# Performance work log

Measured on AMD Instinct MI355X. Metric: run time of the kernel, lower is better.

Reference implementation:

```python
import jax, jax.numpy as jnp
import numpy as np

D_MODEL = 768
D_STATE = 16
D_CONV = 4
EXPAND = 2
D_INNER = D_MODEL * EXPAND
B, L = 2, 2048


def _silu(x):
    return x * jax.nn.sigmoid(x)


def _ssm_core(xn, inw, cw, cb, xw, dtw, dtb, Alog, Dp, outw):
    """Mamba selective SSM. xn: [B,L,d_model] -> [B,L,d_model]."""
    Bn, Ln, _ = xn.shape
    S = Alog.shape[1]
    d_inner = Alog.shape[0]
    k = cw.shape[-1]
    xz = xn @ inw                      # [B,L,2*d_inner]
    xi, z = jnp.split(xz, 2, axis=-1)
    # depthwise causal conv along L (torch pads both sides then slices [:L] == left-pad k-1)
    xc = jnp.swapaxes(xi, 1, 2)        # [B,d_inner,L]
    xc = jax.lax.conv_general_dilated(xc, cw, (1,), [(k - 1, 0)],
                                      feature_group_count=d_inner)
    xc = xc + cb[None, :, None]
    xc = _silu(jnp.swapaxes(xc, 1, 2))  # [B,L,d_inner]
    bcdt = xc @ xw                     # [B,L,1+2S]
    dt_raw = bcdt[..., :1]
    Bs = bcdt[..., 1:1 + S]            # [B,L,S]
    Cs = bcdt[..., 1 + S:]             # [B,L,S]
    dt = jax.nn.softplus(dt_raw * dtw[None, None, :] + dtb)  # [B,L,d_inner]
    A = -jnp.exp(jnp.clip(Alog, -6.0, 6.0))                  # [d_inner,S]
    dA = jnp.exp(dt[..., None] * A[None, None])               # [B,L,d_inner,S]
    dBx = dt[..., None] * Bs[:, :, None, :] * xc[..., None]   # [B,L,d_inner,S]

    def step(h, ins):
        dA_t, dBx_t, C_t = ins
        h = jnp.clip(dA_t * h + dBx_t, -10000.0, 10000.0)
        return h, jnp.einsum('bds,bs->bd', h, C_t)

    h0 = jnp.zeros((Bn, d_inner, S), xc.dtype)
    _, ys = jax.lax.scan(step, h0, (jnp.moveaxis(dA, 1, 0),
                                    jnp.moveaxis(dBx, 1, 0),
                                    jnp.moveaxis(Cs, 1, 0)))
    y = jnp.moveaxis(ys, 0, 1) + xc * Dp[None, None]
    y = y * _silu(z)
    return y @ outw


def setup_inputs() -> dict:
    key = jax.random.key(0)
    ks = jax.random.split(key, 20)
    def core_params(koff):
        return dict(
            inw=jax.random.normal(ks[koff + 0], (D_MODEL, 2 * D_INNER), jnp.float32) * 0.02,
            cw=jax.random.normal(ks[koff + 1], (D_INNER, 1, D_CONV), jnp.float32) * 0.2,
            cb=jnp.zeros((D_INNER,), jnp.float32),
            xw=jax.random.normal(ks[koff + 2], (D_INNER, 1 + 2 * D_STATE), jnp.float32) * 0.02,
            dtw=jax.random.normal(ks[koff + 3], (D_INNER,), jnp.float32) * 0.5,
            dtb=jax.random.normal(ks[koff + 4], (D_INNER,), jnp.float32) * 0.1,
            Alog=jnp.clip(jnp.log(jnp.arange(1, D_STATE + 1, dtype=jnp.float32))[None, :]
                          * jnp.ones((D_INNER, 1), jnp.float32), -6.0, 6.0),
            D=jnp.ones((D_INNER,), jnp.float32),
            outw=jax.random.normal(ks[koff + 5], (D_INNER, D_MODEL), jnp.float32) * 0.02,
        )
    f = core_params(2)
    b = core_params(8)
    return {
        'x': jax.random.normal(ks[0], (B, L, D_MODEL), jnp.float32),
        'ln_g': jnp.ones((D_MODEL,), jnp.float32),
        'ln_b': jnp.zeros((D_MODEL,), jnp.float32),
        'alpha': jnp.zeros((), jnp.float32),
        'f_inw': f['inw'], 'f_cw': f['cw'], 'f_cb': f['cb'], 'f_xw': f['xw'],
        'f_dtw': f['dtw'], 'f_dtb': f['dtb'], 'f_Alog': f['Alog'], 'f_D': f['D'], 'f_outw': f['outw'],
        'b_inw': b['inw'], 'b_cw': b['cw'], 'b_cb': b['cb'], 'b_xw': b['xw'],
        'b_dtw': b['dtw'], 'b_dtb': b['dtb'], 'b_Alog': b['Alog'], 'b_D': b['D'], 'b_outw': b['outw'],
    }


def reference(x, ln_g, ln_b, alpha,
              f_inw, f_cw, f_cb, f_xw, f_dtw, f_dtb, f_Alog, f_D, f_outw,
              b_inw, b_cw, b_cb, b_xw, b_dtw, b_dtb, b_Alog, b_D, b_outw):
    residual = x.astype(jnp.float32)
    mu = residual.mean(-1, keepdims=True)
    var = ((residual - mu) ** 2).mean(-1, keepdims=True)
    xn = (residual - mu) / jnp.sqrt(var + 1e-5) * ln_g + ln_b
    y_fwd = _ssm_core(xn, f_inw, f_cw, f_cb, f_xw, f_dtw, f_dtb, f_Alog, f_D, f_outw)
    y_bwd = jnp.flip(_ssm_core(jnp.flip(xn, 1), b_inw, b_cw, b_cb, b_xw,
                               b_dtw, b_dtb, b_Alog, b_D, b_outw), 1)
    a = jax.nn.sigmoid(alpha)
    y = a * y_fwd + (1.0 - a) * y_bwd
    return y + residual
```

## Files before the change

### kernel.cpp

```cpp
#include <hip/hip_runtime.h>
#include <cstddef>
#include <cstdint>

#define DMODEL 768
#define DINNER 1536
#define NSTATE 16
#define LSEQ   2048
#define NB     2
#define NTOK   (NB*LSEQ)
#define NBCDT  33

#define TC     32
#define NCHUNK (LSEQ/TC)
#define KSPLIT 12
#define LOG2E  1.44269504f

typedef __bf16 bf16x8 __attribute__((ext_vector_type(8)));
typedef float  floatx4 __attribute__((ext_vector_type(4)));

__device__ __forceinline__ float exp2_hw(float x) { return __builtin_amdgcn_exp2f(x); }
__device__ __forceinline__ float silu_f(float x) { return x / (1.f + expf(-x)); }
__device__ __forceinline__ float clip1e4(float x) {
    return __builtin_amdgcn_fmed3f(x, -1e4f, 1e4f);
}
__device__ __forceinline__ unsigned short f2bf(float f) {
    unsigned int u = __float_as_uint(f);
    unsigned int r = u + 0x7fffu + ((u >> 16) & 1u);
    return (unsigned short)(r >> 16);
}
__device__ __forceinline__ float bf2f(unsigned short u) {
    return __uint_as_float((unsigned int)u << 16);
}
__device__ __forceinline__ unsigned int pack2bf(float a, float b) {
    unsigned int ua = __float_as_uint(a); ua = ua + 0x7fffu + ((ua >> 16) & 1u);
    unsigned int ub = __float_as_uint(b); ub = ub + 0x7fffu + ((ub >> 16) & 1u);
    return (ua >> 16) | (ub & 0xffff0000u);
}
__device__ __forceinline__ void ld_lds16(unsigned short* lds, const unsigned short* g) {
    __builtin_amdgcn_global_load_lds(
        (const __attribute__((address_space(1))) unsigned int*)g,
        (__attribute__((address_space(3))) unsigned int*)lds,
        16, 0, 0);
}

__global__ void ln_kernel(const float* __restrict__ x,
                          const float* __restrict__ g,
                          const float* __restrict__ be,
                          unsigned short* __restrict__ xnb,
                          float* __restrict__ bcdt,
                          float* __restrict__ out) {
    int row = blockIdx.x;
    int tid = threadIdx.x;
    int zi = row * 256 + tid;
    if (zi < 2 * NTOK * NBCDT) bcdt[zi] = 0.f;
    const float* xr = x + (size_t)row * DMODEL;
    float s = 0.f, ss = 0.f;
    for (int i = tid; i < DMODEL; i += 256) {
        float v = xr[i];
        s += v; ss += v * v;
    }
    for (int o = 32; o >= 1; o >>= 1) {
        s  += __shfl_xor(s,  o, 64);
        ss += __shfl_xor(ss, o, 64);
    }
    __shared__ float sS[4], sSS[4];
    int w = tid >> 6;
    if ((tid & 63) == 0) { sS[w] = s; sSS[w] = ss; }
    __syncthreads();
    s  = sS[0] + sS[1] + sS[2] + sS[3];
    ss = sSS[0] + sSS[1] + sSS[2] + sSS[3];
    float mu = s / DMODEL;
    float var = ss / DMODEL - mu * mu;
    float rstd = rsqrtf(var + 1e-5f);
    unsigned short* xo = xnb + (size_t)row * DMODEL;
    float* ores = out + (size_t)row * DMODEL;
    for (int i = tid; i < DMODEL; i += 256) {
        float v = xr[i];
        xo[i] = f2bf((v - mu) * rstd * g[i] + be[i]);
        ores[i] = v;
    }
}

__global__ __launch_bounds__(256)
void cast_weights(const float* __restrict__ f_inw, const float* __restrict__ b_inw,
                  const float* __restrict__ f_outw, const float* __restrict__ b_outw,
                  const float* __restrict__ f_xw, const float* __restrict__ b_xw,
                  const float* __restrict__ alpha,
                  unsigned short* __restrict__ inwT, unsigned short* __restrict__ outwT,
                  unsigned short* __restrict__ xwT) {
    __shared__ float t[32][33];
    int bid = blockIdx.x;
    int tid = threadIdx.x;
    int lr = tid >> 5, lc = tid & 31;
    if (bid < 4608) {
        int n0 = (bid % 192) * 32;
        int k0 = (bid / 192) * 32;
        const float* w = (n0 >= 3072) ? b_inw : f_inw;
        int nb = (n0 >= 3072) ? (n0 - 3072) : n0;
        #pragma unroll
        for (int r = 0; r < 4; r++)
            t[r * 8 + lr][lc] = w[(size_t)(k0 + r * 8 + lr) * 3072 + nb + lc];
        __syncthreads();
        #pragma unroll
        for (int r = 0; r < 4; r++)
            inwT[(size_t)(n0 + r * 8 + lr) * DMODEL + k0 + lc] = f2bf(t[lc][r * 8 + lr]);
    } else if (bid < 6912) {
        bid -= 4608;
        float a = 1.f / (1.f + expf(-alpha[0]));
        int n0 = (bid % 24) * 32;
        int k0 = (bid / 24) * 32;
        const float* w = (k0 >= DINNER) ? b_outw : f_outw;
        float sc = (k0 >= DINNER) ? (1.f - a) : a;
        int kb = (k0 >= DINNER) ? (k0 - DINNER) : k0;
        #pragma unroll
        for (int r = 0; r < 4; r++)
            t[r * 8 + lr][lc] = w[(size_t)(kb + r * 8 + lr) * DMODEL + n0 + lc];
        __syncthreads();
        #pragma unroll
        for (int r = 0; r < 4; r++)
            outwT[(size_t)(n0 + r * 8 + lr) * 3072 + k0 + lc] = f2bf(sc * t[lc][r * 8 + lr]);
    } else {
        bid -= 6912;
        int dir = bid / 48;
        int k0 = (bid % 48) * 32;
        const float* xw = dir ? b_xw : f_xw;
        unsigned short* dst = xwT + (size_t)dir * 48 * DINNER;
        for (int idx = tid; idx < 48 * 32; idx += 256) {
            int n = idx >> 5, kk = idx & 31;
            float v = (n < 33) ? xw[(size_t)(k0 + kk) * 33 + n] : 0.f;
            dst[(size_t)n * DINNER + k0 + kk] = f2bf(v);
        }
    }
}

__global__ __launch_bounds__(256)
void gemm_xz_mfma(const unsigned short* __restrict__ xnb,
                  const unsigned short* __restrict__ inwT,
                  unsigned short* __restrict__ xi, unsigned short* __restrict__ sz) {
    __shared__ unsigned short SH[2][2 * 128 * 64];
    int tid = threadIdx.x;
    int bm = blockIdx.y * 128;
    int bn = blockIdx.x * 128;
    int wave = tid >> 6, lane = tid & 63;
    int wm = (wave & 1) * 64, wn = (wave >> 1) * 64;
    int col15 = lane & 15, quad = lane >> 4;
    int lrow = lane >> 3;
    int lk   = (((lane & 7) ^ lrow) * 8);
    floatx4 acc[4][4];
    #pragma unroll
    for (int i = 0; i < 4; i++)
        #pragma unroll
        for (int j = 0; j < 4; j++)
            acc[i][j] = (floatx4){0.f, 0.f, 0.f, 0.f};

    int sw = col15 & 7;

#define STAGE_XZ(buf, k0)                                                       \
    {                                                                           \
        unsigned short* Abuf = SH[buf];                                         \
        unsigned short* Bbuf = SH[buf] + 128 * 64;                              \
        _Pragma("unroll")                                                       \
        for (int i = 0; i < 4; i++) {                                           \
            int r8 = wave * 32 + i * 8;                                         \
            int ra = r8 + lrow;                                                 \
            ld_lds16(&Abuf[r8 * 64], &xnb[(size_t)(bm + ra) * DMODEL + (k0) + lk]); \
            ld_lds16(&Bbuf[r8 * 64], &inwT[(size_t)(bn + ra) * DMODEL + (k0) + lk]); \
        }                                                                       \
    }

    STAGE_XZ(0, 0);
    __syncthreads();
    int cur = 0;
    for (int kt = 0; kt < DMODEL / 64; ++kt) {
        if (kt + 1 < DMODEL / 64) STAGE_XZ(cur ^ 1, (kt + 1) * 64);
        const unsigned short* Acur = SH[cur];
        const unsigned short* Bcur = SH[cur] + 128 * 64;
        #pragma unroll
        for (int k2 = 0; k2 < 2; k2++) {
            bf16x8 af[4], bf_[4];
            int pc = ((k2 * 4 + quad) ^ sw) * 8;
            #pragma unroll
            for (int mt = 0; mt < 4; mt++)
                af[mt] = *(const bf16x8*)(&Acur[(wm + mt * 16 + col15) * 64 + pc]);
            #pragma unroll
            for (int nt = 0; nt < 4; nt++)
                bf_[nt] = *(const bf16x8*)(&Bcur[(wn + nt * 16 + col15) * 64 + pc]);
            #pragma unroll
            for (int mt = 0; mt < 4; mt++)
                #pragma unroll
                for (int nt = 0; nt < 4; nt++)
                    acc[mt][nt] = __builtin_amdgcn_mfma_f32_16x16x32_bf16(
                        af[mt], bf_[nt], acc[mt][nt], 0, 0, 0);
        }
        __syncthreads();
        cur ^= 1;
    }
    int dirq = (bn >= 3072) ? 1 : 0;
    int cb0  = bn - dirq * 3072;
    int zs   = (cb0 >= DINNER) ? 1 : 0;
    int ccb  = cb0 - zs * DINNER;
    unsigned short* dst = zs ? sz : xi;
    unsigned short* C16 = &SH[0][0];
    #pragma unroll
    for (int mt = 0; mt < 4; mt++)
        #pragma unroll
        for (int nt = 0; nt < 4; nt++)
            #pragma unroll
            for (int r = 0; r < 4; r++) {
                int row = wm + mt * 16 + quad * 4 + r;
                int col = wn + nt * 16 + col15;
                float v = acc[mt][nt][r];
                if (zs) v = silu_f(v);
                C16[row * 136 + col] = f2bf(v);
            }
    __syncthreads();
    {
        int erow = tid >> 4;
        int cch  = tid & 15;
        size_t rowbase = (size_t)dirq * NTOK + bm;
        #pragma unroll
        for (int p = 0; p < 8; p++) {
            int row = p * 16 + erow;
            uint4 v = *(const uint4*)(&C16[row * 136 + cch * 8]);
            *(uint4*)(&dst[(rowbase + row) * DINNER + ccb + cch * 8]) = v;
        }
    }
#undef STAGE_XZ
}

__global__ __launch_bounds__(256)
void bcdt_conv_gemm_mfma(const unsigned short* __restrict__ xi,
                         const float* __restrict__ f_cw, const float* __restrict__ f_cb,
                         const float* __restrict__ b_cw, const float* __restrict__ b_cb,
                         const unsigned short* __restrict__ xwT,
                         float* __restrict__ bcdt) {
    __shared__ unsigned short Xs[131 * 64];
    __shared__ unsigned short As[128 * 64];
    __shared__ unsigned short Bs[48 * 64];
    int tid = threadIdx.x;
    int wave = tid >> 6, lane = tid & 63;
    int r0 = blockIdx.x * 128;
    int kc = blockIdx.y;
    int dirb = r0 >> 11;
    int dir = dirb >> 1, b = dirb & 1;
    int u0 = r0 & 2047;
    const float* cw = dir ? b_cw : f_cw;
    const float* cb = dir ? b_cb : f_cb;
    size_t xibase = ((size_t)dir * NTOK + (size_t)b * LSEQ) * DINNER;
    const unsigned short* Bsrc = xwT + (size_t)dir * 48 * DINNER;

    int col15 = lane & 15, quad = lane >> 4;
    int sw = col15 & 7;
    int lrow = lane >> 3;
    int lcc = (lane & 7) * 8;
    int lk  = (((lane & 7) ^ lrow) * 8);
    int wm = wave * 32;

    int cp = (tid & 31) * 2;
    int rg = (tid >> 5) * 16;

    floatx4 acc[2][3];
    #pragma unroll
    for (int i = 0; i < 2; i++)
        #pragma unroll
        for (int j = 0; j < 3; j++)
            acc[i][j] = (floatx4){0.f, 0.f, 0.f, 0.f};

    for (int ks = 0; ks < 2; ks++) {
        int kb = kc * 128 + ks * 64;
        #pragma unroll
        for (int i = 0; i < 2; i++) {
            int g = wave + i * 4;
            if (g < 6)
                ld_lds16(&Bs[g * 8 * 64],
                         &Bsrc[(size_t)(g * 8 + lrow) * DINNER + kb + lk]);
        }
        #pragma unroll
        for (int i = 0; i < 4; i++) {
            int g = wave * 4 + i;
            int u = u0 + g * 8 + lrow;
            int l = dir ? (LSEQ - 1 - u) : u;
            ld_lds16(&Xs[(3 + g * 8) * 64], &xi[xibase + (size_t)l * DINNER + kb + lcc]);
        }
        if (tid < 96) {
            int hh = tid >> 5, c2 = (tid & 31) * 2;
            int u = u0 - 3 + hh;
            unsigned int v = 0;
            if (u >= 0) {
                int l = dir ? (LSEQ - 1 - u) : u;
                v = *(const unsigned int*)(&xi[xibase + (size_t)l * DINNER + kb + c2]);
            }
            *(unsigned int*)(&Xs[hh * 64 + c2]) = v;
        }
        __syncthreads();
        {
            int ch0 = kb + cp;
            float4 w0 = *(const float4*)(cw + (size_t)ch0 * 4);
            float4 w1 = *(const float4*)(cw + (size_t)(ch0 + 1) * 4);
            float cb0 = cb[ch0], cb1 = cb[ch0 + 1];
            unsigned int v;
            v = *(const unsigned int*)(&Xs[(rg + 0) * 64 + cp]);
            float a3 = bf2f((unsigned short)v), b3 = bf2f((unsigned short)(v >> 16));
            v = *(const unsigned int*)(&Xs[(rg + 1) * 64 + cp]);
            float a2 = bf2f((unsigned short)v), b2 = bf2f((unsigned short)(v >> 16));
            v = *(const unsigned int*)(&Xs[(rg + 2) * 64 + cp]);
            float a1 = bf2f((unsigned short)v), b1 = bf2f((unsigned short)(v >> 16));
            int cs = cp >> 3, e = cp & 7;
            #pragma unroll
            for (int j = 0; j < 16; j++) {
                int r = rg + j;
                v = *(const unsigned int*)(&Xs[(r + 3) * 64 + cp]);
                float a0 = bf2f((unsigned short)v), b0 = bf2f((unsigned short)(v >> 16));
                float xa = cb0;
                xa = fmaf(w0.x, a3, xa); xa = fmaf(w0.y, a2, xa);
                xa = fmaf(w0.z, a1, xa); xa = fmaf(w0.w, a0, xa);
                xa = silu_f(xa);
                float xb = cb1;
                xb = fmaf(w1.x, b3, xb); xb = fmaf(w1.y, b2, xb);
                xb = fmaf(w1.z, b1, xb); xb = fmaf(w1.w, b0, xb);
                xb = silu_f(xb);
                a3 = a2; a2 = a1; a1 = a0;
                b3 = b2; b2 = b1; b1 = b0;
                int ad = r * 64 + ((cs ^ (r & 7)) << 3) + e;
                *(unsigned int*)(&As[ad]) = pack2bf(xa, xb);
            }
        }
        __syncthreads();
        #pragma unroll
        for (int k2 = 0; k2 < 2; k2++) {
            int pc = ((k2 * 4 + quad) ^ sw) * 8;
            bf16x8 af[2], bfr[3];
            #pragma unroll
            for (int mt = 0; mt < 2; mt++)
                af[mt] = *(const bf16x8*)(&As[(wm + mt * 16 + col15) * 64 + pc]);
            #pragma unroll
            for (int nt = 0; nt < 3; nt++)
                bfr[nt] = *(const bf16x8*)(&Bs[(nt * 16 + col15) * 64 + pc]);
            #pragma unroll
            for (int mt = 0; mt < 2; mt++)
                #pragma unroll
                for (int nt = 0; nt < 3; nt++)
                    acc[mt][nt] = __builtin_amdgcn_mfma_f32_16x16x32_bf16(
                        af[mt], bfr[nt], acc[mt][nt], 0, 0, 0);
        }
        __syncthreads();
    }
    #pragma unroll
    for (int mt = 0; mt < 2; mt++) {
        #pragma unroll
        for (int nt = 0; nt < 3; nt++) {
            int n = nt * 16 + col15;
            if (n < 33) {
                #pragma unroll
                for (int r = 0; r < 4; r++) {
                    int row = r0 + wm + mt * 16 + quad * 4 + r;
                    atomicAdd(&bcdt[(size_t)row * 33 + n], acc[mt][nt][r]);
                }
            }
        }
    }
}

__global__ __launch_bounds__(256)
void scan_p1(const unsigned short* __restrict__ xi, const float* __restrict__ bcdt,
             const float* __restrict__ f_cw, const float* __restrict__ f_cb,
             const float* __restrict__ b_cw, const float* __restrict__ b_cb,
             const float* __restrict__ f_dtw, const float* __restrict__ f_dtb,
             const float* __restrict__ f_Alog,
             const float* __restrict__ b_dtw, const float* __restrict__ b_dtb,
             const float* __restrict__ b_Alog,
             float* __restrict__ Sdtbuf, float* __restrict__ hloc) {
    int tid = threadIdx.x;
    int d = blockIdx.x * 256 + tid;
    int chunk = blockIdx.y;
    int dirb  = blockIdx.z;
    int dir = dirb >> 1, b = dirb & 1;
    const float* dtw  = dir ? b_dtw  : f_dtw;
    const float* dtb  = dir ? b_dtb  : f_dtb;
    const float* Alog = dir ? b_Alog : f_Alog;
    const float* cw   = dir ? b_cw   : f_cw;
    const float* cb   = dir ? b_cb   : f_cb;
    float dtw_d = dtw[d], dtb_d = dtb[d];
    float4 wc = *(const float4*)(cw + (size_t)d * 4);
    float cb_d = cb[d];
    float A2[NSTATE], h[NSTATE];
    #pragma unroll
    for (int s = 0; s < NSTATE; s++) {
        float al = fminf(fmaxf(Alog[d * NSTATE + s], -6.f), 6.f);
        A2[s] = -__expf(al) * LOG2E;
        h[s] = 0.f;
    }
    float Sdt = 0.f;
    int t0 = chunk * TC;
    size_t xbase = ((size_t)dir * NTOK + (size_t)b * LSEQ) * DINNER + d;
    long stride = dir ? -(long)DINNER : (long)DINNER;
    int l0 = dir ? (LSEQ - 1 - t0) : t0;
    const unsigned short* xp = xi + xbase + (size_t)l0 * DINNER;
    float xm3 = 0.f, xm2 = 0.f, xm1 = 0.f;
    if (chunk) {
        xm3 = bf2f(*(xp - 3 * stride));
        xm2 = bf2f(*(xp - 2 * stride));
        xm1 = bf2f(*(xp - 1 * stride));
    }
    size_t rbase = (size_t)dirb * LSEQ + (size_t)t0;
    const float* bc = bcdt + rbase * NBCDT;
    for (int t = 0; t < TC; t++) {
        float cur = bf2f(*xp); xp += stride;
        float xv = cb_d;
        xv = fmaf(wc.x, xm3, xv);
        xv = fmaf(wc.y, xm2, xv);
        xv = fmaf(wc.z, xm1, xv);
        xv = fmaf(wc.w, cur, xv);
        xv = silu_f(xv);
        xm3 = xm2; xm2 = xm1; xm1 = cur;
        float dt_raw = bc[t * NBCDT];
        float u = fmaf(dt_raw, dtw_d, dtb_d);
        float dt = fmaxf(u, 0.f) + __logf(1.f + __expf(-fabsf(u)));
        Sdt += dt;
        float dtx = dt * xv;
        #pragma unroll
        for (int s = 0; s < NSTATE; s++) {
            float Bv = bc[t * NBCDT + 1 + s];
            h[s] = fmaf(exp2_hw(dt * A2[s]), h[s], dtx * Bv);
        }
    }
    Sdtbuf[(size_t)chunk * (4 * DINNER) + (size_t)dirb * DINNER + d] = Sdt;
    size_t base = ((size_t)chunk * 4 + dirb) * ((size_t)DINNER * NSTATE) + (size_t)d * NSTATE;
    #pragma unroll
    for (int s = 0; s < NSTATE; s++)
        hloc[base + s] = h[s];
}

__global__ void scan_p2(const float* __restrict__ Sdtbuf, const float* __restrict__ hloc,
                        const float* __restrict__ f_Alog, const float* __restrict__ b_Alog,
                        float* __restrict__ hin) {
    int i = blockIdx.x * 256 + threadIdx.x;
    const int DS = DINNER * NSTATE;
    int dirb = i / DS;
    int rem = i - dirb * DS;
    int d = rem >> 4, s = rem & 15;
    const float* Alog = (dirb >> 1) ? b_Alog : f_Alog;
    float al = fminf(fmaxf(Alog[d * NSTATE + s], -6.f), 6.f);
    float A2 = -__expf(al) * LOG2E;
    float h = 0.f;
    const int stride = 4 * DS;
    const int sstr = 4 * DINNER;
    for (int c = 0; c < NCHUNK; c++) {
        size_t idx = (size_t)c * stride + i;
        hin[idx] = h;
        float P = exp2_hw(A2 * Sdtbuf[(size_t)c * sstr + dirb * DINNER + d]);
        h = clip1e4(fmaf(P, h, hloc[idx]));
    }
}

__global__ __launch_bounds__(256)
void scan_p3(const unsigned short* __restrict__ xi, const float* __restrict__ bcdt,
             const unsigned short* __restrict__ sz, const float* __restrict__ hin,
             const float* __restrict__ f_cw, const float* __restrict__ f_cb,
             const float* __restrict__ b_cw, const float* __restrict__ b_cb,
             const float* __restrict__ f_dtw, const float* __restrict__ f_dtb,
             const float* __restrict__ f_Alog, const float* __restrict__ f_D,
             const float* __restrict__ b_dtw, const float* __restrict__ b_dtb,
             const float* __restrict__ b_Alog, const float* __restrict__ b_D,
             unsigned short* __restrict__ yvb) {
    int tid = threadIdx.x;
    int d = blockIdx.x * 256 + tid;
    int chunk = blockIdx.y;
    int dirb  = blockIdx.z;
    int dir = dirb >> 1, b = dirb & 1;
    const float* dtw  = dir ? b_dtw  : f_dtw;
    const float* dtb  = dir ? b_dtb  : f_dtb;
    const float* Alog = dir ? b_Alog : f_Alog;
    const float* Dp   = dir ? b_D    : f_D;
    const float* cw   = dir ? b_cw   : f_cw;
    const float* cb   = dir ? b_cb   : f_cb;
    float dtw_d = dtw[d], dtb_d = dtb[d], D_d = Dp[d];
    float4 wc = *(const float4*)(cw + (size_t)d * 4);
    float cb_d = cb[d];
    float A2[NSTATE], h[NSTATE];
    size_t hbase = ((size_t)chunk * 4 + dirb) * ((size_t)DINNER * NSTATE) + (size_t)d * NSTATE;
    #pragma unroll
    for (int s = 0; s < NSTATE; s++) {
        float al = fminf(fmaxf(Alog[d * NSTATE + s], -6.f), 6.f);
        A2[s] = -__expf(al) * LOG2E;
        h[s] = hin[hbase + s];
    }
    int t0 = chunk * TC;
    size_t xbase = ((size_t)dir * NTOK + (size_t)b * LSEQ) * DINNER + d;
    long stride = dir ? -(long)DINNER : (long)DINNER;
    int l0 = dir ? (LSEQ - 1 - t0) : t0;
    const unsigned short* xp = xi + xbase + (size_t)l0 * DINNER;
    const unsigned short* szp = sz + xbase + (size_t)l0 * DINNER;
    unsigned short* yp = yvb + ((size_t)(b * LSEQ + l0)) * 3072 + dir * DINNER + d;
    long ystride = stride * 2;
    float xm3 = 0.f, xm2 = 0.f, xm1 = 0.f;
    if (chunk) {
        xm3 = bf2f(*(xp - 3 * stride));
        xm2 = bf2f(*(xp - 2 * stride));
        xm1 = bf2f(*(xp - 1 * stride));
    }
    size_t rbase = (size_t)dirb * LSEQ + (size_t)t0;
    const float* bc = bcdt + rbase * NBCDT;
    for (int t = 0; t < TC; t++) {
        float cur = bf2f(*xp); xp += stride;
        float xv = cb_d;
        xv = fmaf(wc.x, xm3, xv);
        xv = fmaf(wc.y, xm2, xv);
        xv = fmaf(wc.z, xm1, xv);
        xv = fmaf(wc.w, cur, xv);
        xv = silu_f(xv);
        xm3 = xm2; xm2 = xm1; xm1 = cur;
        float dt_raw = bc[t * NBCDT];
        float u = fmaf(dt_raw, dtw_d, dtb_d);
        float dt = fmaxf(u, 0.f) + __logf(1.f + __expf(-fabsf(u)));
        float dtx = dt * xv;
        float p = 0.f;
        #pragma unroll
        for (int s = 0; s < NSTATE; s++) {
            float Bv = bc[t * NBCDT + 1 + s];
            float Cv = bc[t * NBCDT + 1 + NSTATE + s];
            h[s] = fmaf(exp2_hw(dt * A2[s]), h[s], dtx * Bv);
            p = fmaf(h[s], Cv, p);
        }
        float szv = bf2f(*szp); szp += stride;
        float y = (p + xv * D_d) * szv;
        *yp = f2bf(y); yp += ystride;
    }
}

__global__ __launch_bounds__(256)
void gemm_out_mfma(const unsigned short* __restrict__ yvb,
                   const unsigned short* __restrict__ outwT,
                   float* __restrict__ out) {
    __shared__ unsigned short SH[2][(128 + 64) * 64];
    int tid = threadIdx.x;
    int bm = blockIdx.y * 128;
    int bn = blockIdx.x * 64;
    int ks = blockIdx.z;
    int wave = tid >> 6, lane = tid & 63;
    int wm = (wave & 1) * 64, wn = (wave >> 1) * 32;
    int col15 = lane & 15, quad = lane >> 4;
    int lrow = lane >> 3;
    int lk   = (((lane & 7) ^ lrow) * 8);
    floatx4 acc[4][2];
    #pragma unroll
    for (int i = 0; i < 4; i++)
        #pragma unroll
        for (int j = 0; j < 2; j++)
            acc[i][j] = (floatx4){0.f, 0.f, 0.f, 0.f};

    int sw = col15 & 7;
    int kbase = ks * DINNER;

#define STAGE_OUT(buf, k0)                                                      \
    {                                                                           \
        unsigned short* Abuf = SH[buf];                                         \
        unsigned short* Bbuf = SH[buf] + 128 * 64;                              \
        _Pragma("unroll")                                                       \
        for (int i = 0; i < 4; i++) {                                           \
            int r8 = wave * 32 + i * 8;                                         \
            ld_lds16(&Abuf[r8 * 64], &yvb[(size_t)(bm + r8 + lrow) * 3072 + (k0) + lk]); \
        }                                                                       \
        _Pragma("unroll")                                                       \
        for (int i = 0; i < 2; i++) {                                           \
            int r8 = wave * 16 + i * 8;                                         \
            ld_lds16(&Bbuf[r8 * 64], &outwT[(size_t)(bn + r8 + lrow) * 3072 + (k0) + lk]); \
        }                                                                       \
    }

    STAGE_OUT(0, kbase);
    __syncthreads();
    int cur = 0;
    for (int kt = 0; kt < DINNER / 64; ++kt) {
        if (kt + 1 < DINNER / 64) STAGE_OUT(cur ^ 1, kbase + (kt + 1) * 64);
        const unsigned short* Acur = SH[cur];
        const unsigned short* Bcur = SH[cur] + 128 * 64;
        #pragma unroll
        for (int k2 = 0; k2 < 2; k2++) {
            bf16x8 af[4], bf_[2];
            int pc = ((k2 * 4 + quad) ^ sw) * 8;
            #pragma unroll
            for (int mt = 0; mt < 4; mt++)
                af[mt] = *(const bf16x8*)(&Acur[(wm + mt * 16 + col15) * 64 + pc]);
            #pragma unroll
            for (int nt = 0; nt < 2; nt++)
                bf_[nt] = *(const bf16x8*)(&Bcur[(wn + nt * 16 + col15) * 64 + pc]);
            #pragma unroll
            for (int mt = 0; mt < 4; mt++)
                #pragma unroll
                for (int nt = 0; nt < 2; nt++)
                    acc[mt][nt] = __builtin_amdgcn_mfma_f32_16x16x32_bf16(
                        af[mt], bf_[nt], acc[mt][nt], 0, 0, 0);
        }
        __syncthreads();
        cur ^= 1;
    }
    #pragma unroll
    for (int mt = 0; mt < 4; mt++) {
        #pragma unroll
        for (int nt = 0; nt < 2; nt++) {
            #pragma unroll
            for (int r = 0; r < 4; r++) {
                int row = bm + wm + mt * 16 + quad * 4 + r;
                int gn  = bn + wn + nt * 16 + col15;
                atomicAdd(&out[(size_t)row * DMODEL + gn], acc[mt][nt][r]);
            }
        }
    }
#undef STAGE_OUT
}

extern "C" void kernel_launch(void* const* d_in, const int* in_sizes, int n_in,
                              void* d_out, int out_size, void* d_ws, size_t ws_size,
                              hipStream_t stream) {
    const float* x     = (const float*)d_in[0];
    const float* ln_g  = (const float*)d_in[1];
    const float* ln_b  = (const float*)d_in[2];
    const float* alpha = (const float*)d_in[3];
    const float* f_inw  = (const float*)d_in[4];
    const float* f_cw   = (const float*)d_in[5];
    const float* f_cb   = (const float*)d_in[6];
    const float* f_xw   = (const float*)d_in[7];
    const float* f_dtw  = (const float*)d_in[8];
    const float* f_dtb  = (const float*)d_in[9];
    const float* f_Alog = (const float*)d_in[10];
    const float* f_D    = (const float*)d_in[11];
    const float* f_outw = (const float*)d_in[12];
    const float* b_inw  = (const float*)d_in[13];
    const float* b_cw   = (const float*)d_in[14];
    const float* b_cb   = (const float*)d_in[15];
    const float* b_xw   = (const float*)d_in[16];
    const float* b_dtw  = (const float*)d_in[17];
    const float* b_dtb  = (const float*)d_in[18];
    const float* b_Alog = (const float*)d_in[19];
    const float* b_D    = (const float*)d_in[20];
    const float* b_outw = (const float*)d_in[21];
    float* out = (float*)d_out;

    float* ws = (float*)d_ws;
    float* r_xnb  = ws;
    float* r_inwT = r_xnb + 1572864;
    float* r_outwT= r_inwT + 2359296;
    float* r_xib  = r_outwT + 1179648;
    float* r_szb  = r_xib + 6291456;
    float* r_yvb  = r_szb + 6291456;
    float* hloc   = r_yvb + 6291456;
    float* hin    = hloc + 6291456;
    float* Sdtbuf = hin + 6291456;
    float* bcdt   = Sdtbuf + 393216;

    unsigned short* xnb   = (unsigned short*)r_xnb;
    unsigned short* inwT  = (unsigned short*)r_inwT;
    unsigned short* outwT = (unsigned short*)r_outwT;
    unsigned short* xib   = (unsigned short*)r_xib;
    unsigned short* szb   = (unsigned short*)r_szb;
    unsigned short* yvb   = (unsigned short*)r_yvb;
    unsigned short* xwT   = (unsigned short*)hloc;

    ln_kernel<<<NTOK, 256, 0, stream>>>(x, ln_g, ln_b, xnb, bcdt, out);
    cast_weights<<<4608 + 2304 + 96, 256, 0, stream>>>(f_inw, b_inw, f_outw, b_outw,
                                                       f_xw, b_xw, alpha,
                                                       inwT, outwT, xwT);
    {
        dim3 grid(6144 / 128, NTOK / 128);
        gemm_xz_mfma<<<grid, 256, 0, stream>>>(xnb, inwT, xib, szb);
    }
    {
        dim3 g(2 * NTOK / 128, KSPLIT);
        bcdt_conv_gemm_mfma<<<g, 256, 0, stream>>>(xib, f_cw, f_cb, b_cw, b_cb,
                                                   xwT, bcdt);
    }
    {
        dim3 grid1(DINNER / 256, NCHUNK, 4);
        scan_p1<<<grid1, 256, 0, stream>>>(xib, bcdt, f_cw, f_cb, b_cw, b_cb,
                                           f_dtw, f_dtb, f_Alog,
                                           b_dtw, b_dtb, b_Alog, Sdtbuf, hloc);
        scan_p2<<<(4 * DINNER * NSTATE) / 256, 256, 0, stream>>>(Sdtbuf, hloc,
                                                                 f_Alog, b_Alog, hin);
        scan_p3<<<grid1, 256, 0, stream>>>(xib, bcdt, szb, hin,
                                           f_cw, f_cb, b_cw, b_cb,
                                           f_dtw, f_dtb, f_Alog, f_D,
                                           b_dtw, b_dtb, b_Alog, b_D, yvb);
    }
    {
        dim3 grid(DMODEL / 64, NTOK / 128, 2);
        gemm_out_mfma<<<grid, 256, 0, stream>>>(yvb, outwT, out);
    }
}
```

Before: 398.3 us.

## Materialize conv output once, drop split-K atomics, fold residual into out GEMM

The bcdt GEMM kernel now writes the conv+SiLU activations to a new bf16 buffer, so both scan passes read it directly instead of recomputing the depthwise conv and SiLU per chunk. scan_p2 updates hloc in place, which removes the separate hin buffer. The output GEMM drops its K-split atomics: it uses 64-row tiles over the full 3072 K range and writes out = acc + x directly, so the LN kernel no longer copies the residual. The scans also get launch bounds for occupancy. The trade-off is an extra 25 MB write and read of xc and a longer serial K loop per output block.

```diff
diff --git a/kernel.cpp b/kernel.cpp
--- a/kernel.cpp
+++ b/kernel.cpp
@@ -47,8 +47,7 @@
                           const float* __restrict__ g,
                           const float* __restrict__ be,
                           unsigned short* __restrict__ xnb,
-                          float* __restrict__ bcdt,
-                          float* __restrict__ out) {
+                          float* __restrict__ bcdt) {
     int row = blockIdx.x;
     int tid = threadIdx.x;
     int zi = row * 256 + tid;
@@ -73,12 +72,8 @@
     float var = ss / DMODEL - mu * mu;
     float rstd = rsqrtf(var + 1e-5f);
     unsigned short* xo = xnb + (size_t)row * DMODEL;
-    float* ores = out + (size_t)row * DMODEL;
-    for (int i = tid; i < DMODEL; i += 256) {
-        float v = xr[i];
-        xo[i] = f2bf((v - mu) * rstd * g[i] + be[i]);
-        ores[i] = v;
-    }
+    for (int i = tid; i < DMODEL; i += 256)
+        xo[i] = f2bf((xr[i] - mu) * rstd * g[i] + be[i]);
 }
 
 __global__ __launch_bounds__(256)
@@ -233,7 +228,8 @@
                          const float* __restrict__ f_cw, const float* __restrict__ f_cb,
                          const float* __restrict__ b_cw, const float* __restrict__ b_cb,
                          const unsigned short* __restrict__ xwT,
-                         float* __restrict__ bcdt) {
+                         float* __restrict__ bcdt,
+                         unsigned short* __restrict__ xc) {
     __shared__ unsigned short Xs[131 * 64];
     __shared__ unsigned short As[128 * 64];
     __shared__ unsigned short Bs[48 * 64];
@@ -248,6 +244,7 @@
     const float* cb = dir ? b_cb : f_cb;
     size_t xibase = ((size_t)dir * NTOK + (size_t)b * LSEQ) * DINNER;
     const unsigned short* Bsrc = xwT + (size_t)dir * 48 * DINNER;
+    unsigned short* xcb = xc + (size_t)dirb * LSEQ * DINNER;
 
     int col15 = lane & 15, quad = lane >> 4;
     int sw = col15 & 7;
@@ -321,8 +318,10 @@
                 xb = silu_f(xb);
                 a3 = a2; a2 = a1; a1 = a0;
                 b3 = b2; b2 = b1; b1 = b0;
+                unsigned int pk = pack2bf(xa, xb);
                 int ad = r * 64 + ((cs ^ (r & 7)) << 3) + e;
-                *(unsigned int*)(&As[ad]) = pack2bf(xa, xb);
+                *(unsigned int*)(&As[ad]) = pk;
+                *(unsigned int*)(&xcb[(size_t)(u0 + r) * DINNER + ch0]) = pk;
             }
         }
         __syncthreads();
@@ -361,10 +360,8 @@
     }
 }
 
-__global__ __launch_bounds__(256)
-void scan_p1(const unsigned short* __restrict__ xi, const float* __restrict__ bcdt,
-             const float* __restrict__ f_cw, const float* __restrict__ f_cb,
-             const float* __restrict__ b_cw, const float* __restrict__ b_cb,
+__global__ __launch_bounds__(256, 4)
+void scan_p1(const unsigned short* __restrict__ xc, const float* __restrict__ bcdt,
              const float* __restrict__ f_dtw, const float* __restrict__ f_dtb,
              const float* __restrict__ f_Alog,
              const float* __restrict__ b_dtw, const float* __restrict__ b_dtb,
@@ -374,15 +371,11 @@
     int d = blockIdx.x * 256 + tid;
     int chunk = blockIdx.y;
     int dirb  = blockIdx.z;
-    int dir = dirb >> 1, b = dirb & 1;
+    int dir = dirb >> 1;
     const float* dtw  = dir ? b_dtw  : f_dtw;
     const float* dtb  = dir ? b_dtb  : f_dtb;
     const float* Alog = dir ? b_Alog : f_Alog;
-    const float* cw   = dir ? b_cw   : f_cw;
-    const float* cb   = dir ? b_cb   : f_cb;
     float dtw_d = dtw[d], dtb_d = dtb[d];
-    float4 wc = *(const float4*)(cw + (size_t)d * 4);
-    float cb_d = cb[d];
     float A2[NSTATE], h[NSTATE];
     #pragma unroll
     for (int s = 0; s < NSTATE; s++) {
@@ -392,27 +385,11 @@
     }
     float Sdt = 0.f;
     int t0 = chunk * TC;
-    size_t xbase = ((size_t)dir * NTOK + (size_t)b * LSEQ) * DINNER + d;
-    long stride = dir ? -(long)DINNER : (long)DINNER;
-    int l0 = dir ? (LSEQ - 1 - t0) : t0;
-    const unsigned short* xp = xi + xbase + (size_t)l0 * DINNER;
-    float xm3 = 0.f, xm2 = 0.f, xm1 = 0.f;
-    if (chunk) {
-        xm3 = bf2f(*(xp - 3 * stride));
-        xm2 = bf2f(*(xp - 2 * stride));
-        xm1 = bf2f(*(xp - 1 * stride));
-    }
+    const unsigned short* xp = xc + ((size_t)dirb * LSEQ + t0) * DINNER + d;
     size_t rbase = (size_t)dirb * LSEQ + (size_t)t0;
     const float* bc = bcdt + rbase * NBCDT;
     for (int t = 0; t < TC; t++) {
-        float cur = bf2f(*xp); xp += stride;
-        float xv = cb_d;
-        xv = fmaf(wc.x, xm3, xv);
-        xv = fmaf(wc.y, xm2, xv);
-        xv = fmaf(wc.z, xm1, xv);
-        xv = fmaf(wc.w, cur, xv);
-        xv = silu_f(xv);
-        xm3 = xm2; xm2 = xm1; xm1 = cur;
+        float xv = bf2f(*xp); xp += DINNER;
         float dt_raw = bc[t * NBCDT];
         float u = fmaf(dt_raw, dtw_d, dtb_d);
         float dt = fmaxf(u, 0.f) + __logf(1.f + __expf(-fabsf(u)));
@@ -431,9 +408,8 @@
         hloc[base + s] = h[s];
 }
 
-__global__ void scan_p2(const float* __restrict__ Sdtbuf, const float* __restrict__ hloc,
-                        const float* __restrict__ f_Alog, const float* __restrict__ b_Alog,
-                        float* __restrict__ hin) {
+__global__ void scan_p2(const float* __restrict__ Sdtbuf, float* __restrict__ hloc,
+                        const float* __restrict__ f_Alog, const float* __restrict__ b_Alog) {
     int i = blockIdx.x * 256 + threadIdx.x;
     const int DS = DINNER * NSTATE;
     int dirb = i / DS;
@@ -447,17 +423,16 @@
     const int sstr = 4 * DINNER;
     for (int c = 0; c < NCHUNK; c++) {
         size_t idx = (size_t)c * stride + i;
-        hin[idx] = h;
+        float tmp = hloc[idx];
+        hloc[idx] = h;
         float P = exp2_hw(A2 * Sdtbuf[(size_t)c * sstr + dirb * DINNER + d]);
-        h = clip1e4(fmaf(P, h, hloc[idx]));
-    }
-}
-
-__global__ __launch_bounds__(256)
-void scan_p3(const unsigned short* __restrict__ xi, const float* __restrict__ bcdt,
-             const unsigned short* __restrict__ sz, const float* __restrict__ hin,
-             const float* __restrict__ f_cw, const float* __restrict__ f_cb,
-             const float* __restrict__ b_cw, const float* __restrict__ b_cb,
+        h = clip1e4(fmaf(P, h, tmp));
+    }
+}
+
+__global__ __launch_bounds__(256, 4)
+void scan_p3(const unsigned short* __restrict__ xc, const float* __restrict__ bcdt,
+             const unsigned short* __restrict__ sz, const float* __restrict__ hpre,
              const float* __restrict__ f_dtw, const float* __restrict__ f_dtb,
              const float* __restrict__ f_Alog, const float* __restrict__ f_D,
              const float* __restrict__ b_dtw, const float* __restrict__ b_dtb,
@@ -472,44 +447,27 @@
     const float* dtb  = dir ? b_dtb  : f_dtb;
     const float* Alog = dir ? b_Alog : f_Alog;
     const float* Dp   = dir ? b_D    : f_D;
-    const float* cw   = dir ? b_cw   : f_cw;
-    const float* cb   = dir ? b_cb   : f_cb;
     float dtw_d = dtw[d], dtb_d = dtb[d], D_d = Dp[d];
-    float4 wc = *(const float4*)(cw + (size_t)d * 4);
-    float cb_d = cb[d];
     float A2[NSTATE], h[NSTATE];
     size_t hbase = ((size_t)chunk * 4 + dirb) * ((size_t)DINNER * NSTATE) + (size_t)d * NSTATE;
     #pragma unroll
     for (int s = 0; s < NSTATE; s++) {
         float al = fminf(fmaxf(Alog[d * NSTATE + s], -6.f), 6.f);
         A2[s] = -__expf(al) * LOG2E;
-        h[s] = hin[hbase + s];
+        h[s] = hpre[hbase + s];
     }
     int t0 = chunk * TC;
+    const unsigned short* xp = xc + ((size_t)dirb * LSEQ + t0) * DINNER + d;
     size_t xbase = ((size_t)dir * NTOK + (size_t)b * LSEQ) * DINNER + d;
     long stride = dir ? -(long)DINNER : (long)DINNER;
     int l0 = dir ? (LSEQ - 1 - t0) : t0;
-    const unsigned short* xp = xi + xbase + (size_t)l0 * DINNER;
     const unsigned short* szp = sz + xbase + (size_t)l0 * DINNER;
     unsigned short* yp = yvb + ((size_t)(b * LSEQ + l0)) * 3072 + dir * DINNER + d;
     long ystride = stride * 2;
-    float xm3 = 0.f, xm2 = 0.f, xm1 = 0.f;
-    if (chunk) {
-        xm3 = bf2f(*(xp - 3 * stride));
-        xm2 = bf2f(*(xp - 2 * stride));
-        xm1 = bf2f(*(xp - 1 * stride));
-    }
     size_t rbase = (size_t)dirb * LSEQ + (size_t)t0;
     const float* bc = bcdt + rbase * NBCDT;
     for (int t = 0; t < TC; t++) {
-        float cur = bf2f(*xp); xp += stride;
-        float xv = cb_d;
-        xv = fmaf(wc.x, xm3, xv);
-        xv = fmaf(wc.y, xm2, xv);
-        xv = fmaf(wc.z, xm1, xv);
-        xv = fmaf(wc.w, cur, xv);
-        xv = silu_f(xv);
-        xm3 = xm2; xm2 = xm1; xm1 = cur;
+        float xv = bf2f(*xp); xp += DINNER;
         float dt_raw = bc[t * NBCDT];
         float u = fmaf(dt_raw, dtw_d, dtb_d);
         float dt = fmaxf(u, 0.f) + __logf(1.f + __expf(-fabsf(u)));
@@ -531,62 +489,57 @@
 __global__ __launch_bounds__(256)
 void gemm_out_mfma(const unsigned short* __restrict__ yvb,
                    const unsigned short* __restrict__ outwT,
+                   const float* __restrict__ x,
                    float* __restrict__ out) {
-    __shared__ unsigned short SH[2][(128 + 64) * 64];
+    __shared__ unsigned short SH[2][2 * 64 * 64];
     int tid = threadIdx.x;
-    int bm = blockIdx.y * 128;
+    int bm = blockIdx.y * 64;
     int bn = blockIdx.x * 64;
-    int ks = blockIdx.z;
     int wave = tid >> 6, lane = tid & 63;
-    int wm = (wave & 1) * 64, wn = (wave >> 1) * 32;
+    int wm = (wave & 1) * 32, wn = (wave >> 1) * 32;
     int col15 = lane & 15, quad = lane >> 4;
     int lrow = lane >> 3;
     int lk   = (((lane & 7) ^ lrow) * 8);
-    floatx4 acc[4][2];
-    #pragma unroll
-    for (int i = 0; i < 4; i++)
+    floatx4 acc[2][2];
+    #pragma unroll
+    for (int i = 0; i < 2; i++)
         #pragma unroll
         for (int j = 0; j < 2; j++)
             acc[i][j] = (floatx4){0.f, 0.f, 0.f, 0.f};
 
     int sw = col15 & 7;
-    int kbase = ks * DINNER;
 
 #define STAGE_OUT(buf, k0)                                                      \
     {                                                                           \
         unsigned short* Abuf = SH[buf];                                         \
-        unsigned short* Bbuf = SH[buf] + 128 * 64;                              \
-        _Pragma("unroll")                                                       \
-        for (int i = 0; i < 4; i++) {                                           \
-            int r8 = wave * 32 + i * 8;                                         \
-            ld_lds16(&Abuf[r8 * 64], &yvb[(size_t)(bm + r8 + lrow) * 3072 + (k0) + lk]); \
-        }                                                                       \
+        unsigned short* Bbuf = SH[buf] + 64 * 64;                               \
         _Pragma("unroll")                                                       \
         for (int i = 0; i < 2; i++) {                                           \
             int r8 = wave * 16 + i * 8;                                         \
+            ld_lds16(&Abuf[r8 * 64], &yvb[(size_t)(bm + r8 + lrow) * 3072 + (k0) + lk]); \
             ld_lds16(&Bbuf[r8 * 64], &outwT[(size_t)(bn + r8 + lrow) * 3072 + (k0) + lk]); \
         }                                                                       \
     }
 
-    STAGE_OUT(0, kbase);
+    STAGE_OUT(0, 0);
     __syncthreads();
     int cur = 0;
-    for (int kt = 0; kt < DINNER / 64; ++kt) {
-        if (kt + 1 < DINNER / 64) STAGE_OUT(cur ^ 1, kbase + (kt + 1) * 64);
+    for (int kt = 0; kt < 3072 / 64; ++kt) {
+        if (kt + 1 < 3072 / 64) STAGE_OUT(cur ^ 1, (kt + 1) * 64);
         const unsigned short* Acur = SH[cur];
-        const unsigned short* Bcur = SH[cur] + 128 * 64;
+        const unsigned short* Bcur = SH[cur] + 64 * 64;
         #pragma unroll
         for (int k2 = 0; k2 < 2; k2++) {
-            bf16x8 af[4], bf_[2];
+            bf16x8 af[2], bf_[2];
             int pc = ((k2 * 4 + quad) ^ sw) * 8;
             #pragma unroll
-            for (int mt = 0; mt < 4; mt++)
+            for (int mt = 0; mt < 2; mt++)
                 af[mt] = *(const bf16x8*)(&Acur[(wm + mt * 16 + col15) * 64 + pc]);
             #pragma unroll
             for (int nt = 0; nt < 2; nt++)
                 bf_[nt] = *(const bf16x8*)(&Bcur[(wn + nt * 16 + col15) * 64 + pc]);
             #pragma unroll
-            for (int mt = 0; mt < 4; mt++)
+            for (int mt = 0; mt < 2; mt++)
                 #pragma unroll
                 for (int nt = 0; nt < 2; nt++)
                     acc[mt][nt] = __builtin_amdgcn_mfma_f32_16x16x32_bf16(
@@ -596,14 +549,14 @@
         cur ^= 1;
     }
     #pragma unroll
-    for (int mt = 0; mt < 4; mt++) {
+    for (int mt = 0; mt < 2; mt++) {
         #pragma unroll
         for (int nt = 0; nt < 2; nt++) {
             #pragma unroll
             for (int r = 0; r < 4; r++) {
                 int row = bm + wm + mt * 16 + quad * 4 + r;
                 int gn  = bn + wn + nt * 16 + col15;
-                atomicAdd(&out[(size_t)row * DMODEL + gn], acc[mt][nt][r]);
+                out[(size_t)row * DMODEL + gn] = acc[mt][nt][r] + x[(size_t)row * DMODEL + gn];
             }
         }
     }
@@ -645,8 +598,8 @@
     float* r_szb  = r_xib + 6291456;
     float* r_yvb  = r_szb + 6291456;
     float* hloc   = r_yvb + 6291456;
-    float* hin    = hloc + 6291456;
-    float* Sdtbuf = hin + 6291456;
+    float* r_xc   = hloc + 6291456;
+    float* Sdtbuf = r_xc + 6291456;
     float* bcdt   = Sdtbuf + 393216;
 
     unsigned short* xnb   = (unsigned short*)r_xnb;
@@ -655,9 +608,10 @@
     unsigned short* xib   = (unsigned short*)r_xib;
     unsigned short* szb   = (unsigned short*)r_szb;
     unsigned short* yvb   = (unsigned short*)r_yvb;
+    unsigned short* xcb   = (unsigned short*)r_xc;
     unsigned short* xwT   = (unsigned short*)hloc;
 
-    ln_kernel<<<NTOK, 256, 0, stream>>>(x, ln_g, ln_b, xnb, bcdt, out);
+    ln_kernel<<<NTOK, 256, 0, stream>>>(x, ln_g, ln_b, xnb, bcdt);
     cast_weights<<<4608 + 2304 + 96, 256, 0, stream>>>(f_inw, b_inw, f_outw, b_outw,
                                                        f_xw, b_xw, alpha,
                                                        inwT, outwT, xwT);
@@ -668,22 +622,21 @@
     {
         dim3 g(2 * NTOK / 128, KSPLIT);
         bcdt_conv_gemm_mfma<<<g, 256, 0, stream>>>(xib, f_cw, f_cb, b_cw, b_cb,
-                                                   xwT, bcdt);
+                                                   xwT, bcdt, xcb);
     }
     {
         dim3 grid1(DINNER / 256, NCHUNK, 4);
-        scan_p1<<<grid1, 256, 0, stream>>>(xib, bcdt, f_cw, f_cb, b_cw, b_cb,
+        scan_p1<<<grid1, 256, 0, stream>>>(xcb, bcdt,
                                            f_dtw, f_dtb, f_Alog,
                                            b_dtw, b_dtb, b_Alog, Sdtbuf, hloc);
         scan_p2<<<(4 * DINNER * NSTATE) / 256, 256, 0, stream>>>(Sdtbuf, hloc,
-                                                                 f_Alog, b_Alog, hin);
-        scan_p3<<<grid1, 256, 0, stream>>>(xib, bcdt, szb, hin,
-                                           f_cw, f_cb, b_cw, b_cb,
+                                                                 f_Alog, b_Alog);
+        scan_p3<<<grid1, 256, 0, stream>>>(xcb, bcdt, szb, hloc,
                                            f_dtw, f_dtb, f_Alog, f_D,
                                            b_dtw, b_dtb, b_Alog, b_D, yvb);
     }
     {
-        dim3 grid(DMODEL / 64, NTOK / 128, 2);
-        gemm_out_mfma<<<grid, 256, 0, stream>>>(yvb, outwT, out);
-    }
-}
+        dim3 grid(DMODEL / 64, NTOK / 64);
+        gemm_out_mfma<<<grid, 256, 0, stream>>>(yvb, outwT, x, out);
+    }
+}
```

Measured after the change: 361.3 us. -9.3%, faster.
